# Optimization experiments

Hardware: AMD Instinct MI355X
Metric: run time of the kernel (lower is better)

Reference implementation:

```python
import jax, jax.numpy as jnp
import numpy as np

B, S, C, H = 2, 4096, 1024, 16
DH = C // H  # 64
# diffusers: attn.scale = dim_head ** -0.5; code divides scores by scale**0.5
SCALE = 1.0 / (float(DH) ** -0.25)  # == DH ** 0.25


def setup_inputs() -> dict:
    key = jax.random.key(0)
    ks = jax.random.split(key, 6)
    w = 0.02
    return {
        "hidden_states": jax.random.normal(ks[0], (B, S, C), jnp.float32),
        "Wq": jax.random.normal(ks[1], (C, C), jnp.float32) * w,
        "Wk": jax.random.normal(ks[2], (C, C), jnp.float32) * w,
        "Wv": jax.random.normal(ks[3], (C, C), jnp.float32) * w,
        "Wo": jax.random.normal(ks[4], (C, C), jnp.float32) * w,
        "bo": jnp.zeros((C,), jnp.float32),
        # token sizes >= 1 (number of patches each token represents)
        "token_sizes": jax.random.randint(ks[5], (B, S), 1, 17, jnp.int32),
    }


def _split_heads(x):
    # [B, S, C] -> [B, H, S, DH]
    return x.reshape(B, S, H, DH).transpose(0, 2, 1, 3)


def reference(hidden_states, Wq, Wk, Wv, Wo, bo, token_sizes):
    q = _split_heads(hidden_states @ Wq)  # [B,H,S,DH]
    k = _split_heads(hidden_states @ Wk)
    v = _split_heads(hidden_states @ Wv)
    # QK^T with diffusers-style scaling: scores / attn.scale**0.5 == scores * DH**0.25
    scores = jnp.einsum("bhqd,bhkd->bhqk", q, k) * SCALE  # [B,H,S,S]
    # additive log(token_size) bias over keys (self-attention path)
    log_sizes = jnp.log(token_sizes.astype(jnp.float32))  # [B,S]
    scores = scores + log_sizes[:, None, None, :]
    probs = jax.nn.softmax(scores, axis=-1)
    out = jnp.einsum("bhqk,bhkd->bhqd", probs, v)  # [B,H,S,DH]
    out = out.transpose(0, 2, 1, 3).reshape(B, S, C)  # merge heads
    return out @ Wo + bo  # to_out[0] linear; to_out[1] dropout is identity
```

## Files before the change

### kernel.cpp

```cpp
#include <hip/hip_runtime.h>


typedef unsigned short u16;
typedef unsigned int u32;
typedef _Float16 f16x8 __attribute__((ext_vector_type(8)));
typedef float f32x4 __attribute__((ext_vector_type(4)));
typedef short short4v __attribute__((ext_vector_type(4)));

constexpr int SEQ = 4096, CDIM = 1024, NH = 16, DHE = 64;
constexpr float SCALE2 = 2.8284271247461903f * 1.4426950408889634f;

union Frag { f16x8 v; short4v h[2]; };

__device__ __forceinline__ u16 f2h(float f) {
  union { _Float16 h; u16 u; } x;
  x.h = (_Float16)f;
  return x.u;
}

__device__ __forceinline__ u32 pkrtz(float a, float b) {
  u32 r;
  asm("v_cvt_pkrtz_f16_f32 %0, %1, %2" : "=v"(r) : "v"(a), "v"(b));
  return r;
}

__device__ __forceinline__ short4v pk4(const f32x4& v) {
  union { u32 w[2]; short4v s; } u;
  u.w[0] = pkrtz(v[0], v[1]);
  u.w[1] = pkrtz(v[2], v[3]);
  return u.s;
}

__device__ __forceinline__ float exp2fast(float x) {
  float r;
  asm("v_exp_f32 %0, %1" : "=v"(r) : "v"(x));
  return r;
}

__device__ __forceinline__ f32x4 mfma16(const Frag& a, const Frag& b, f32x4 c) {
  return __builtin_amdgcn_mfma_f32_16x16x32_f16(a.v, b.v, c, 0, 0, 0);
}


__global__ void cast_x_kernel(const float* __restrict__ x, u16* __restrict__ out) {
  size_t i = ((size_t)blockIdx.x * 256 + threadIdx.x) * 8;
  float4 a = *(const float4*)(x + i);
  float4 b = *(const float4*)(x + i + 4);
  uint4 o;
  o.x = (u32)f2h(a.x) | ((u32)f2h(a.y) << 16);
  o.y = (u32)f2h(a.z) | ((u32)f2h(a.w) << 16);
  o.z = (u32)f2h(b.x) | ((u32)f2h(b.y) << 16);
  o.w = (u32)f2h(b.z) | ((u32)f2h(b.w) << 16);
  *(uint4*)(out + i) = o;
}

__global__ __launch_bounds__(256) void transpose_w4_kernel(
    const float* __restrict__ Wq, const float* __restrict__ Wk,
    const float* __restrict__ Wv, const float* __restrict__ Wo,
    u16* __restrict__ dq, u16* __restrict__ dk,
    u16* __restrict__ dv, u16* __restrict__ dow) {
  __shared__ float tile[64][65];
  const float* src;
  u16* dst;
  switch (blockIdx.z) {
    case 0: src = Wq; dst = dq; break;
    case 1: src = Wk; dst = dk; break;
    case 2: src = Wv; dst = dv; break;
    default: src = Wo; dst = dow; break;
  }
  const int r0 = blockIdx.y * 64, c0 = blockIdx.x * 64;
  const int tx = threadIdx.x & 63, ty = threadIdx.x >> 6;
#pragma unroll
  for (int i = 0; i < 16; ++i) {
    const int row = i * 4 + ty;
    tile[row][tx] = src[(size_t)(r0 + row) * 1024 + c0 + tx];
  }
  __syncthreads();
#pragma unroll
  for (int i = 0; i < 16; ++i) {
    const int row = i * 4 + ty;
    dst[(size_t)(c0 + row) * 1024 + r0 + tx] = f2h(tile[tx][row]);
  }
}

__global__ void tscast_kernel(const int* __restrict__ ts, u16* __restrict__ out) {
  int i = blockIdx.x * 256 + threadIdx.x;
  out[i] = f2h((float)ts[i]);
}


template <int EPI>
__global__ __launch_bounds__(256) void gemm_f16(const u16* __restrict__ A,
                                                const u16* __restrict__ Bt,
                                                void* __restrict__ Out,
                                                const float* __restrict__ bias,
                                                const int* __restrict__ ts) {
  __shared__ __align__(16) short Alds[128][40];
  __shared__ __align__(16) short Blds[128][40];
  const int t = threadIdx.x;
  const int bnb = blockIdx.x;
  const int bm = blockIdx.y;
  const int lane = t & 63, wv = t >> 6;
  const int wm = wv >> 1, wn = wv & 1;
  const int l16 = lane & 15, lq = lane >> 4;

  f32x4 acc[4][4];
  f32x4 z = {0.f, 0.f, 0.f, 0.f};
#pragma unroll
  for (int i = 0; i < 4; ++i)
#pragma unroll
    for (int j = 0; j < 4; ++j) acc[i][j] = z;

  const int srow = (t * 8) >> 5;
  const int scol = (t * 8) & 31;

  for (int kb = 0; kb < 32; ++kb) {
    const int k0 = kb * 32;
#pragma unroll
    for (int i = 0; i < 2; ++i) {
      const int row = srow + i * 64;
      uint4 va = *(const uint4*)(A + (size_t)(bm * 128 + row) * 1024 + k0 + scol);
      *(uint4*)&Alds[row][scol] = va;
      uint4 vb = *(const uint4*)(Bt + (size_t)(bnb * 128 + row) * 1024 + k0 + scol);
      *(uint4*)&Blds[row][scol] = vb;
    }
    __syncthreads();

    Frag af[4], bf[4];
#pragma unroll
    for (int am = 0; am < 4; ++am) {
      const short* p = &Alds[wm * 64 + am * 16 + l16][lq * 4];
      af[am].h[0] = *(const short4v*)p;
      af[am].h[1] = *(const short4v*)(p + 16);
    }
#pragma unroll
    for (int bn = 0; bn < 4; ++bn) {
      const short* p = &Blds[wn * 64 + bn * 16 + l16][lq * 4];
      bf[bn].h[0] = *(const short4v*)p;
      bf[bn].h[1] = *(const short4v*)(p + 16);
    }
#pragma unroll
    for (int am = 0; am < 4; ++am)
#pragma unroll
      for (int bn = 0; bn < 4; ++bn) acc[am][bn] = mfma16(af[am], bf[bn], acc[am][bn]);
    __syncthreads();
  }

#pragma unroll
  for (int am = 0; am < 4; ++am) {
#pragma unroll
    for (int bn = 0; bn < 4; ++bn) {
#pragma unroll
      for (int r = 0; r < 4; ++r) {
        const int m = bm * 128 + wm * 64 + am * 16 + lq * 4 + r;
        const int n = bnb * 128 + wn * 64 + bn * 16 + l16;
        float vsum = acc[am][bn][r];
        if (EPI == 0) {
          const int which = n >> 10;
          const int nn = n & 1023;
          const int h = nn >> 6, d = nn & 63;
          const int b = m >> 12, s = m & 4095;
          const int bhh = b * NH + h;
          size_t addr;
          if (which == 2) {
            vsum *= (float)ts[b * SEQ + s];
            addr = (size_t)2 * 8388608 + ((size_t)bhh * DHE + d) * SEQ + s;
          } else {
            if (which == 0) vsum *= SCALE2;
            addr = (size_t)which * 8388608 + ((size_t)bhh * SEQ + s) * DHE + d;
          }
          ((u16*)Out)[addr] = f2h(vsum);
        } else {
          ((float*)Out)[(size_t)m * 1024 + n] = vsum + bias[n];
        }
      }
    }
  }
}


__global__ __launch_bounds__(256, 2) void attn_kernel(const u16* __restrict__ Q,
                                                      const u16* __restrict__ K,
                                                      const u16* __restrict__ Vt,
                                                      const u16* __restrict__ ts16,
                                                      u16* __restrict__ Out) {
  __shared__ __align__(16) short Klds[2][64][72];
  __shared__ __align__(16) short Vtlds[2][64][72];

  const int t = threadIdx.x;
  const int bh = blockIdx.x >> 4;
  const int qb = blockIdx.x & 15;
  const int lane = t & 63, wv = t >> 6;
  const int l16 = lane & 15, lq = lane >> 4;
  const int b = bh >> 4, h = bh & 15;

  Frag qf[4][2];
#pragma unroll
  for (int qh = 0; qh < 4; ++qh) {
    const int qrow = qb * 256 + wv * 64 + qh * 16 + l16;
    const u16* qp = Q + ((size_t)bh * SEQ + qrow) * DHE;
#pragma unroll
    for (int f = 0; f < 2; ++f) {
      qf[qh][f].h[0] = *(const short4v*)(qp + f * 32 + lq * 4);
      qf[qh][f].h[1] = *(const short4v*)(qp + f * 32 + lq * 4 + 16);
    }
  }

  float mrow[4] = {0.f, 0.f, 0.f, 0.f};
  f32x4 lsum[4];
  f32x4 oacc[4][4];
  f32x4 z = {0.f, 0.f, 0.f, 0.f};
#pragma unroll
  for (int qh = 0; qh < 4; ++qh) {
    lsum[qh] = z;
#pragma unroll
    for (int d = 0; d < 4; ++d) oacc[qh][d] = z;
  }

  const int a7 = t & 7, sd = a7 * 8, skey = t >> 3;
  const int vd = t >> 2, voct = (t & 3) * 8;
  const int vsw = ((vd >> 3) & 7) << 3;

  const u16* Kbase = K + (size_t)bh * SEQ * DHE;
  const u16* Vtbase = Vt + ((size_t)bh * DHE + vd) * SEQ;
  const u16* tsb = ts16 + b * SEQ;

  uint4 kv0 = *(const uint4*)(Kbase + (size_t)skey * DHE + sd);
  uint4 kv1 = *(const uint4*)(Kbase + (size_t)(skey + 32) * DHE + sd);
  uint4 vv0 = *(const uint4*)(Vtbase + voct);
  uint4 vv1 = *(const uint4*)(Vtbase + voct + 32);

  for (int kt = 0; kt < 64; ++kt) {
    short (*Kb)[72] = Klds[kt & 1];
    short (*Vb)[72] = Vtlds[kt & 1];
    *(uint4*)&Kb[skey][sd] = kv0;
    *(uint4*)&Kb[skey + 32][sd] = kv1;
    *(uint4*)&Vb[vd][voct ^ vsw] = vv0;
    *(uint4*)&Vb[vd][(voct + 32) ^ vsw] = vv1;

    if (kt < 63) {
      const u16* Kn = Kbase + (size_t)(kt + 1) * 64 * DHE + (size_t)skey * DHE + sd;
      kv0 = *(const uint4*)(Kn);
      kv1 = *(const uint4*)(Kn + 32 * DHE);
      const u16* Vn = Vtbase + (kt + 1) * 64 + voct;
      vv0 = *(const uint4*)(Vn);
      vv1 = *(const uint4*)(Vn + 32);
    }
    __syncthreads();

    Frag tsfr[2];
    {
      const u16* tst = tsb + kt * 64;
#pragma unroll
      for (int kh = 0; kh < 2; ++kh) {
        tsfr[kh].h[0] = *(const short4v*)(tst + kh * 32 + lq * 4);
        tsfr[kh].h[1] = *(const short4v*)(tst + kh * 32 + lq * 4 + 16);
      }
    }

    Frag kfr[4][2];
#pragma unroll
    for (int k2 = 0; k2 < 4; ++k2) {
#pragma unroll
      for (int f = 0; f < 2; ++f) {
        const short* p = &Kb[k2 * 16 + l16][f * 32 + lq * 4];
        kfr[k2][f].h[0] = *(const short4v*)p;
        kfr[k2][f].h[1] = *(const short4v*)(p + 16);
      }
    }

    Frag paf[4][2];
#pragma unroll
    for (int qh = 0; qh < 4; ++qh) {
      f32x4 seed;
      {
        const float nm = -mrow[qh];
        seed[0] = nm; seed[1] = nm; seed[2] = nm; seed[3] = nm;
      }
      f32x4 sc[4];
#pragma unroll
      for (int k2 = 0; k2 < 4; ++k2) {
        f32x4 a = mfma16(kfr[k2][0], qf[qh][0], seed);
        a = mfma16(kfr[k2][1], qf[qh][1], a);
        sc[k2] = a;
      }
      float hm[4];
#pragma unroll
      for (int k2 = 0; k2 < 4; ++k2) {
        const f32x4 s = sc[k2];
        hm[k2] = fmaxf(fmaxf(s[0], s[1]), fmaxf(s[2], s[3]));
      }
      float mx = fmaxf(fmaxf(hm[0], hm[1]), fmaxf(hm[2], hm[3]));
      mx = fmaxf(mx, __shfl_xor(mx, 16));
      mx = fmaxf(mx, __shfl_xor(mx, 32));
      if (__any(mx > 8.f)) {
        const float sh = fmaxf(mx, 0.f);
        const float al = exp2fast(-sh);
        mrow[qh] += sh;
        f32x4 alv;
#pragma unroll
        for (int r = 0; r < 4; ++r) alv[r] = __shfl(al, lq * 4 + r, 16);
#pragma unroll
        for (int dd = 0; dd < 4; ++dd) oacc[qh][dd] *= alv;
        lsum[qh] *= alv;
#pragma unroll
        for (int k2 = 0; k2 < 4; ++k2) sc[k2] -= sh;
      }
#pragma unroll
      for (int k2 = 0; k2 < 4; ++k2) {
        f32x4 s = sc[k2];
#pragma unroll
        for (int r = 0; r < 4; ++r) s[r] = exp2fast(s[r]);
        sc[k2] = s;
      }
      paf[qh][0].h[0] = pk4(sc[0]); paf[qh][0].h[1] = pk4(sc[1]);
      paf[qh][1].h[0] = pk4(sc[2]); paf[qh][1].h[1] = pk4(sc[3]);
      lsum[qh] = mfma16(paf[qh][0], tsfr[0], lsum[qh]);
      lsum[qh] = mfma16(paf[qh][1], tsfr[1], lsum[qh]);
    }

    __builtin_amdgcn_s_setprio(1);
#pragma unroll
    for (int dd = 0; dd < 4; ++dd) {
      const int vrow = dd * 16 + l16;
      const int e = ((vrow >> 3) & 7) << 3;
#pragma unroll
      for (int kh = 0; kh < 2; ++kh) {
        Frag vb;
        vb.h[0] = *(const short4v*)&Vb[vrow][(kh * 32 + lq * 4) ^ e];
        vb.h[1] = *(const short4v*)&Vb[vrow][(kh * 32 + 16 + lq * 4) ^ e];
#pragma unroll
        for (int qh = 0; qh < 4; ++qh)
          oacc[qh][dd] = mfma16(paf[qh][kh], vb, oacc[qh][dd]);
      }
    }
    __builtin_amdgcn_s_setprio(0);
  }

#pragma unroll
  for (int qh = 0; qh < 4; ++qh) {
    f32x4 linv;
#pragma unroll
    for (int r = 0; r < 4; ++r) linv[r] = 1.f / lsum[qh][r];
#pragma unroll
    for (int dd = 0; dd < 4; ++dd) {
#pragma unroll
      for (int r = 0; r < 4; ++r) {
        const int row = qb * 256 + wv * 64 + qh * 16 + lq * 4 + r;
        const float v = oacc[qh][dd][r] * linv[r];
        Out[((size_t)b * SEQ + row) * CDIM + h * DHE + dd * 16 + l16] = f2h(v);
      }
    }
  }
}


extern "C" void kernel_launch(void* const* d_in, const int* in_sizes, int n_in,
                              void* d_out, int out_size, void* d_ws, size_t ws_size,
                              hipStream_t stream) {
  const float* hs = (const float*)d_in[0];
  const float* Wq = (const float*)d_in[1];
  const float* Wk = (const float*)d_in[2];
  const float* Wv = (const float*)d_in[3];
  const float* Wo = (const float*)d_in[4];
  const float* bo = (const float*)d_in[5];
  const int* ts = (const int*)d_in[6];
  float* out = (float*)d_out;

  char* ws = (char*)d_ws;
  u16* xf = (u16*)(ws);
  u16* wtq = (u16*)(ws + 16777216);
  u16* wtk = (u16*)(ws + 18874368);
  u16* wtv = (u16*)(ws + 20971520);
  u16* wto = (u16*)(ws + 23068672);
  u16* qbuf = (u16*)(ws + 25165824);
  u16* kbuf = (u16*)(ws + 41943040);
  u16* vtbuf = (u16*)(ws + 58720256);
  u16* ts16 = (u16*)(ws + 75497472);

  cast_x_kernel<<<4096, 256, 0, stream>>>(hs, xf);
  transpose_w4_kernel<<<dim3(16, 16, 4), 256, 0, stream>>>(Wq, Wk, Wv, Wo,
                                                           wtq, wtk, wtv, wto);
  tscast_kernel<<<32, 256, 0, stream>>>(ts, ts16);

  gemm_f16<0><<<dim3(24, 64), 256, 0, stream>>>(xf, wtq, (void*)qbuf, nullptr, ts);

  attn_kernel<<<512, 256, 0, stream>>>(qbuf, kbuf, vtbuf, ts16, xf);

  gemm_f16<1><<<dim3(8, 64), 256, 0, stream>>>(xf, wto, (void*)out, bo, nullptr);

  (void)in_sizes; (void)n_in; (void)out_size; (void)ws_size;
}
```

Measured before the change: 339.5 us.

## Use direct global-to-LDS loads with XOR swizzle and interleave QK/softmax-PV

Replaces register-staged global loads with global_load_lds DMA directly into unpadded, XOR-swizzled shared memory in both the projection GEMM and the attention kernel, which removes VGPR staging and the LDS write instructions. The attention loop is restructured to issue the next tile's DMA after the barrier. It also interleaves the QK MFMAs of one query group with the softmax and PV work of the previous group to overlap matrix and vector work. V fragments are now reloaded per query group, adding LDS reads, and the GEMM has no double buffering, so its loads stay exposed.

```diff
diff --git a/kernel.cpp b/kernel.cpp
--- a/kernel.cpp
+++ b/kernel.cpp
@@ -10,6 +10,8 @@
 constexpr int SEQ = 4096, CDIM = 1024, NH = 16, DHE = 64;
 constexpr float SCALE2 = 2.8284271247461903f * 1.4426950408889634f;
 
+template <int N> struct IC { static constexpr int v = N; };
+
 union Frag { f16x8 v; short4v h[2]; };
 
 __device__ __forceinline__ u16 f2h(float f) {
@@ -39,6 +41,12 @@
 
 __device__ __forceinline__ f32x4 mfma16(const Frag& a, const Frag& b, f32x4 c) {
   return __builtin_amdgcn_mfma_f32_16x16x32_f16(a.v, b.v, c, 0, 0, 0);
+}
+
+__device__ __forceinline__ void gl16(const void* g, void* l) {
+  __builtin_amdgcn_global_load_lds(
+      (const __attribute__((address_space(1))) u32*)g,
+      (__attribute__((address_space(3))) u32*)l, 16, 0, 0);
 }
 
 
@@ -95,8 +103,8 @@
                                                 void* __restrict__ Out,
                                                 const float* __restrict__ bias,
                                                 const int* __restrict__ ts) {
-  __shared__ __align__(16) short Alds[128][40];
-  __shared__ __align__(16) short Blds[128][40];
+  __shared__ __align__(16) short Alds[128 * 32];
+  __shared__ __align__(16) short Blds[128 * 32];
   const int t = threadIdx.x;
   const int bnb = blockIdx.x;
   const int bm = blockIdx.y;
@@ -111,33 +119,37 @@
 #pragma unroll
     for (int j = 0; j < 4; ++j) acc[i][j] = z;
 
-  const int srow = (t * 8) >> 5;
-  const int scol = (t * 8) & 31;
+  const int srow = t >> 2;
+  const int schunk = (t & 3) ^ ((t >> 3) & 3);
+  const u16* Ag = A + (size_t)(bm * 128 + srow) * 1024 + schunk * 8;
+  const u16* Bg = Bt + (size_t)(bnb * 128 + srow) * 1024 + schunk * 8;
+  short* Ad = Alds + (t >> 6) * 512;
+  short* Bd = Blds + (t >> 6) * 512;
+
+  const int m2 = (l16 >> 1) & 3;
+  const int o0 = (((lq >> 1) ^ m2) * 8) + (lq & 1) * 4;
+  const int o1 = ((((lq >> 1) | 2) ^ m2) * 8) + (lq & 1) * 4;
 
   for (int kb = 0; kb < 32; ++kb) {
     const int k0 = kb * 32;
-#pragma unroll
-    for (int i = 0; i < 2; ++i) {
-      const int row = srow + i * 64;
-      uint4 va = *(const uint4*)(A + (size_t)(bm * 128 + row) * 1024 + k0 + scol);
-      *(uint4*)&Alds[row][scol] = va;
-      uint4 vb = *(const uint4*)(Bt + (size_t)(bnb * 128 + row) * 1024 + k0 + scol);
-      *(uint4*)&Blds[row][scol] = vb;
-    }
+    gl16(Ag + k0, Ad);
+    gl16(Ag + 64 * 1024 + k0, Ad + 2048);
+    gl16(Bg + k0, Bd);
+    gl16(Bg + 64 * 1024 + k0, Bd + 2048);
     __syncthreads();
 
     Frag af[4], bf[4];
 #pragma unroll
     for (int am = 0; am < 4; ++am) {
-      const short* p = &Alds[wm * 64 + am * 16 + l16][lq * 4];
-      af[am].h[0] = *(const short4v*)p;
-      af[am].h[1] = *(const short4v*)(p + 16);
+      const short* p = Alds + (wm * 64 + am * 16 + l16) * 32;
+      af[am].h[0] = *(const short4v*)(p + o0);
+      af[am].h[1] = *(const short4v*)(p + o1);
     }
 #pragma unroll
     for (int bn = 0; bn < 4; ++bn) {
-      const short* p = &Blds[wn * 64 + bn * 16 + l16][lq * 4];
-      bf[bn].h[0] = *(const short4v*)p;
-      bf[bn].h[1] = *(const short4v*)(p + 16);
+      const short* p = Blds + (wn * 64 + bn * 16 + l16) * 32;
+      bf[bn].h[0] = *(const short4v*)(p + o0);
+      bf[bn].h[1] = *(const short4v*)(p + o1);
     }
 #pragma unroll
     for (int am = 0; am < 4; ++am)
@@ -184,8 +196,8 @@
                                                       const u16* __restrict__ Vt,
                                                       const u16* __restrict__ ts16,
                                                       u16* __restrict__ Out) {
-  __shared__ __align__(16) short Klds[2][64][72];
-  __shared__ __align__(16) short Vtlds[2][64][72];
+  __shared__ __align__(16) short Klds[2][64 * 64];
+  __shared__ __align__(16) short Vlds[2][64 * 64];
 
   const int t = threadIdx.x;
   const int bh = blockIdx.x >> 4;
@@ -194,6 +206,25 @@
   const int l16 = lane & 15, lq = lane >> 4;
   const int b = bh >> 4, h = bh & 15;
 
+  const int arow = t >> 3;
+  const int achunk = (t & 7) ^ ((t >> 3) & 7);
+  const u16* Kg = K + ((size_t)bh * SEQ + arow) * DHE + achunk * 8;
+  const u16* Vg = Vt + ((size_t)bh * DHE + arow) * SEQ + achunk * 8;
+  const u16* tsb = ts16 + b * SEQ;
+
+  auto stage = [&](int tile, int bufi) {
+    short* Kd = &Klds[bufi][0] + (t >> 6) * 512;
+    short* Vd = &Vlds[bufi][0] + (t >> 6) * 512;
+    const u16* ks = Kg + (size_t)tile * 64 * 64;
+    const u16* vs = Vg + tile * 64;
+    gl16(ks, Kd);
+    gl16(ks + 32 * 64, Kd + 2048);
+    gl16(vs, Vd);
+    gl16(vs + (size_t)32 * SEQ, Vd + 2048);
+  };
+
+  stage(0, 0);
+
   Frag qf[4][2];
 #pragma unroll
   for (int qh = 0; qh < 4; ++qh) {
@@ -217,38 +248,84 @@
     for (int d = 0; d < 4; ++d) oacc[qh][d] = z;
   }
 
-  const int a7 = t & 7, sd = a7 * 8, skey = t >> 3;
-  const int vd = t >> 2, voct = (t & 3) * 8;
-  const int vsw = ((vd >> 3) & 7) << 3;
-
-  const u16* Kbase = K + (size_t)bh * SEQ * DHE;
-  const u16* Vtbase = Vt + ((size_t)bh * DHE + vd) * SEQ;
-  const u16* tsb = ts16 + b * SEQ;
-
-  uint4 kv0 = *(const uint4*)(Kbase + (size_t)skey * DHE + sd);
-  uint4 kv1 = *(const uint4*)(Kbase + (size_t)(skey + 32) * DHE + sd);
-  uint4 vv0 = *(const uint4*)(Vtbase + voct);
-  uint4 vv1 = *(const uint4*)(Vtbase + voct + 32);
+  const int m8 = l16 & 7;
+  const int sA = lq >> 1;
+  const int w4 = (lq & 1) * 4;
+  auto fr_ld = [&](Frag& fr, const short* base, int row, int fk) {
+    const short* p = base + row * 64;
+    const int sl = fk * 4 + sA;
+    fr.h[0] = *(const short4v*)(p + ((sl ^ m8) * 8 + w4));
+    fr.h[1] = *(const short4v*)(p + (((sl | 2) ^ m8) * 8 + w4));
+  };
+
+  Frag tsfr[2];
+
+  auto qk = [&](auto qc, Frag (&kf)[4][2], f32x4 (&dst)[4]) {
+    constexpr int qh = decltype(qc)::v;
+    const float nm = -mrow[qh];
+    f32x4 seed = {nm, nm, nm, nm};
+#pragma unroll
+    for (int k2 = 0; k2 < 4; ++k2) {
+      f32x4 a = mfma16(kf[k2][0], qf[qh][0], seed);
+      dst[k2] = mfma16(kf[k2][1], qf[qh][1], a);
+    }
+  };
+
+  auto smpv = [&](auto qc, const short* Vb, f32x4 (&sc)[4]) {
+    constexpr int qh = decltype(qc)::v;
+    float hm[4];
+#pragma unroll
+    for (int k2 = 0; k2 < 4; ++k2) {
+      const f32x4 s = sc[k2];
+      hm[k2] = fmaxf(fmaxf(s[0], s[1]), fmaxf(s[2], s[3]));
+    }
+    float mx = fmaxf(fmaxf(hm[0], hm[1]), fmaxf(hm[2], hm[3]));
+    mx = fmaxf(mx, __shfl_xor(mx, 16));
+    mx = fmaxf(mx, __shfl_xor(mx, 32));
+    if (__any(mx > 8.f)) {
+      const float sh = fmaxf(mx, 0.f);
+      const float al = exp2fast(-sh);
+      mrow[qh] += sh;
+      f32x4 alv;
+#pragma unroll
+      for (int r = 0; r < 4; ++r) alv[r] = __shfl(al, lq * 4 + r, 16);
+#pragma unroll
+      for (int dd = 0; dd < 4; ++dd) oacc[qh][dd] *= alv;
+      lsum[qh] *= alv;
+#pragma unroll
+      for (int k2 = 0; k2 < 4; ++k2) sc[k2] -= sh;
+    }
+#pragma unroll
+    for (int k2 = 0; k2 < 4; ++k2) {
+      f32x4 s = sc[k2];
+#pragma unroll
+      for (int r = 0; r < 4; ++r) s[r] = exp2fast(s[r]);
+      sc[k2] = s;
+    }
+    Frag paf0, paf1;
+    paf0.h[0] = pk4(sc[0]); paf0.h[1] = pk4(sc[1]);
+    paf1.h[0] = pk4(sc[2]); paf1.h[1] = pk4(sc[3]);
+    __builtin_amdgcn_s_setprio(1);
+    lsum[qh] = mfma16(paf0, tsfr[0], lsum[qh]);
+    lsum[qh] = mfma16(paf1, tsfr[1], lsum[qh]);
+#pragma unroll
+    for (int dd = 0; dd < 4; ++dd) {
+      Frag vb0, vb1;
+      fr_ld(vb0, Vb, dd * 16 + l16, 0);
+      fr_ld(vb1, Vb, dd * 16 + l16, 1);
+      oacc[qh][dd] = mfma16(paf0, vb0, oacc[qh][dd]);
+      oacc[qh][dd] = mfma16(paf1, vb1, oacc[qh][dd]);
+    }
+    __builtin_amdgcn_s_setprio(0);
+  };
+
+  f32x4 scA[4], scB[4];
 
   for (int kt = 0; kt < 64; ++kt) {
-    short (*Kb)[72] = Klds[kt & 1];
-    short (*Vb)[72] = Vtlds[kt & 1];
-    *(uint4*)&Kb[skey][sd] = kv0;
-    *(uint4*)&Kb[skey + 32][sd] = kv1;
-    *(uint4*)&Vb[vd][voct ^ vsw] = vv0;
-    *(uint4*)&Vb[vd][(voct + 32) ^ vsw] = vv1;
-
-    if (kt < 63) {
-      const u16* Kn = Kbase + (size_t)(kt + 1) * 64 * DHE + (size_t)skey * DHE + sd;
-      kv0 = *(const uint4*)(Kn);
-      kv1 = *(const uint4*)(Kn + 32 * DHE);
-      const u16* Vn = Vtbase + (kt + 1) * 64 + voct;
-      vv0 = *(const uint4*)(Vn);
-      vv1 = *(const uint4*)(Vn + 32);
-    }
     __syncthreads();
-
-    Frag tsfr[2];
+    const short* Kb = &Klds[kt & 1][0];
+    const short* Vb = &Vlds[kt & 1][0];
+
     {
       const u16* tst = tsb + kt * 64;
 #pragma unroll
@@ -257,84 +334,20 @@
         tsfr[kh].h[1] = *(const short4v*)(tst + kh * 32 + lq * 4 + 16);
       }
     }
+    if (kt < 63) stage(kt + 1, (kt + 1) & 1);
 
     Frag kfr[4][2];
 #pragma unroll
     for (int k2 = 0; k2 < 4; ++k2) {
-#pragma unroll
-      for (int f = 0; f < 2; ++f) {
-        const short* p = &Kb[k2 * 16 + l16][f * 32 + lq * 4];
-        kfr[k2][f].h[0] = *(const short4v*)p;
-        kfr[k2][f].h[1] = *(const short4v*)(p + 16);
-      }
-    }
-
-    Frag paf[4][2];
-#pragma unroll
-    for (int qh = 0; qh < 4; ++qh) {
-      f32x4 seed;
-      {
-        const float nm = -mrow[qh];
-        seed[0] = nm; seed[1] = nm; seed[2] = nm; seed[3] = nm;
-      }
-      f32x4 sc[4];
-#pragma unroll
-      for (int k2 = 0; k2 < 4; ++k2) {
-        f32x4 a = mfma16(kfr[k2][0], qf[qh][0], seed);
-        a = mfma16(kfr[k2][1], qf[qh][1], a);
-        sc[k2] = a;
-      }
-      float hm[4];
-#pragma unroll
-      for (int k2 = 0; k2 < 4; ++k2) {
-        const f32x4 s = sc[k2];
-        hm[k2] = fmaxf(fmaxf(s[0], s[1]), fmaxf(s[2], s[3]));
-      }
-      float mx = fmaxf(fmaxf(hm[0], hm[1]), fmaxf(hm[2], hm[3]));
-      mx = fmaxf(mx, __shfl_xor(mx, 16));
-      mx = fmaxf(mx, __shfl_xor(mx, 32));
-      if (__any(mx > 8.f)) {
-        const float sh = fmaxf(mx, 0.f);
-        const float al = exp2fast(-sh);
-        mrow[qh] += sh;
-        f32x4 alv;
-#pragma unroll
-        for (int r = 0; r < 4; ++r) alv[r] = __shfl(al, lq * 4 + r, 16);
-#pragma unroll
-        for (int dd = 0; dd < 4; ++dd) oacc[qh][dd] *= alv;
-        lsum[qh] *= alv;
-#pragma unroll
-        for (int k2 = 0; k2 < 4; ++k2) sc[k2] -= sh;
-      }
-#pragma unroll
-      for (int k2 = 0; k2 < 4; ++k2) {
-        f32x4 s = sc[k2];
-#pragma unroll
-        for (int r = 0; r < 4; ++r) s[r] = exp2fast(s[r]);
-        sc[k2] = s;
-      }
-      paf[qh][0].h[0] = pk4(sc[0]); paf[qh][0].h[1] = pk4(sc[1]);
-      paf[qh][1].h[0] = pk4(sc[2]); paf[qh][1].h[1] = pk4(sc[3]);
-      lsum[qh] = mfma16(paf[qh][0], tsfr[0], lsum[qh]);
-      lsum[qh] = mfma16(paf[qh][1], tsfr[1], lsum[qh]);
-    }
-
-    __builtin_amdgcn_s_setprio(1);
-#pragma unroll
-    for (int dd = 0; dd < 4; ++dd) {
-      const int vrow = dd * 16 + l16;
-      const int e = ((vrow >> 3) & 7) << 3;
-#pragma unroll
-      for (int kh = 0; kh < 2; ++kh) {
-        Frag vb;
-        vb.h[0] = *(const short4v*)&Vb[vrow][(kh * 32 + lq * 4) ^ e];
-        vb.h[1] = *(const short4v*)&Vb[vrow][(kh * 32 + 16 + lq * 4) ^ e];
-#pragma unroll
-        for (int qh = 0; qh < 4; ++qh)
-          oacc[qh][dd] = mfma16(paf[qh][kh], vb, oacc[qh][dd]);
-      }
-    }
-    __builtin_amdgcn_s_setprio(0);
+      fr_ld(kfr[k2][0], Kb, k2 * 16 + l16, 0);
+      fr_ld(kfr[k2][1], Kb, k2 * 16 + l16, 1);
+    }
+
+    qk(IC<0>{}, kfr, scA);
+    qk(IC<1>{}, kfr, scB);  smpv(IC<0>{}, Vb, scA);
+    qk(IC<2>{}, kfr, scA);  smpv(IC<1>{}, Vb, scB);
+    qk(IC<3>{}, kfr, scB);  smpv(IC<2>{}, Vb, scA);
+    smpv(IC<3>{}, Vb, scB);
   }
 
 #pragma unroll
```

Result: slower. 374.8 us (+10.4%).

## Use direct global-to-LDS loads in GEMM and interleave QK/softmax per query block

Applied to the files above, without the earlier changes.

The projection GEMM now loads A/B tiles straight into LDS with global_load_lds and a packed, XOR-swizzled layout, replacing register staging and padded rows. Fragment reads use matching swizzled offsets to avoid bank conflicts. In attention, the per-query-block QK MFMAs and softmax are split into lambdas and software-pipelined across two score buffers, so the next block's MFMAs can overlap the current block's exp/max work. This adds register pressure from the second score buffer, and correctness relies on the swizzle mapping matching between writes and reads.

```diff
diff --git a/kernel.cpp b/kernel.cpp
--- a/kernel.cpp
+++ b/kernel.cpp
@@ -10,6 +10,8 @@
 constexpr int SEQ = 4096, CDIM = 1024, NH = 16, DHE = 64;
 constexpr float SCALE2 = 2.8284271247461903f * 1.4426950408889634f;
 
+template <int N> struct IC { static constexpr int v = N; };
+
 union Frag { f16x8 v; short4v h[2]; };
 
 __device__ __forceinline__ u16 f2h(float f) {
@@ -39,6 +41,12 @@
 
 __device__ __forceinline__ f32x4 mfma16(const Frag& a, const Frag& b, f32x4 c) {
   return __builtin_amdgcn_mfma_f32_16x16x32_f16(a.v, b.v, c, 0, 0, 0);
+}
+
+__device__ __forceinline__ void gl16(const void* g, void* l) {
+  __builtin_amdgcn_global_load_lds(
+      (const __attribute__((address_space(1))) u32*)g,
+      (__attribute__((address_space(3))) u32*)l, 16, 0, 0);
 }
 
 
@@ -95,8 +103,8 @@
                                                 void* __restrict__ Out,
                                                 const float* __restrict__ bias,
                                                 const int* __restrict__ ts) {
-  __shared__ __align__(16) short Alds[128][40];
-  __shared__ __align__(16) short Blds[128][40];
+  __shared__ __align__(16) short Alds[128 * 32];
+  __shared__ __align__(16) short Blds[128 * 32];
   const int t = threadIdx.x;
   const int bnb = blockIdx.x;
   const int bm = blockIdx.y;
@@ -111,33 +119,37 @@
 #pragma unroll
     for (int j = 0; j < 4; ++j) acc[i][j] = z;
 
-  const int srow = (t * 8) >> 5;
-  const int scol = (t * 8) & 31;
+  const int srow = t >> 2;
+  const int schunk = (t & 3) ^ ((t >> 3) & 3);
+  const u16* Ag = A + (size_t)(bm * 128 + srow) * 1024 + schunk * 8;
+  const u16* Bg = Bt + (size_t)(bnb * 128 + srow) * 1024 + schunk * 8;
+  short* Ad = Alds + (t >> 6) * 512;
+  short* Bd = Blds + (t >> 6) * 512;
+
+  const int m2 = (l16 >> 1) & 3;
+  const int o0 = (((lq >> 1) ^ m2) * 8) + (lq & 1) * 4;
+  const int o1 = ((((lq >> 1) | 2) ^ m2) * 8) + (lq & 1) * 4;
 
   for (int kb = 0; kb < 32; ++kb) {
     const int k0 = kb * 32;
-#pragma unroll
-    for (int i = 0; i < 2; ++i) {
-      const int row = srow + i * 64;
-      uint4 va = *(const uint4*)(A + (size_t)(bm * 128 + row) * 1024 + k0 + scol);
-      *(uint4*)&Alds[row][scol] = va;
-      uint4 vb = *(const uint4*)(Bt + (size_t)(bnb * 128 + row) * 1024 + k0 + scol);
-      *(uint4*)&Blds[row][scol] = vb;
-    }
+    gl16(Ag + k0, Ad);
+    gl16(Ag + 64 * 1024 + k0, Ad + 2048);
+    gl16(Bg + k0, Bd);
+    gl16(Bg + 64 * 1024 + k0, Bd + 2048);
     __syncthreads();
 
     Frag af[4], bf[4];
 #pragma unroll
     for (int am = 0; am < 4; ++am) {
-      const short* p = &Alds[wm * 64 + am * 16 + l16][lq * 4];
-      af[am].h[0] = *(const short4v*)p;
-      af[am].h[1] = *(const short4v*)(p + 16);
+      const short* p = Alds + (wm * 64 + am * 16 + l16) * 32;
+      af[am].h[0] = *(const short4v*)(p + o0);
+      af[am].h[1] = *(const short4v*)(p + o1);
     }
 #pragma unroll
     for (int bn = 0; bn < 4; ++bn) {
-      const short* p = &Blds[wn * 64 + bn * 16 + l16][lq * 4];
-      bf[bn].h[0] = *(const short4v*)p;
-      bf[bn].h[1] = *(const short4v*)(p + 16);
+      const short* p = Blds + (wn * 64 + bn * 16 + l16) * 32;
+      bf[bn].h[0] = *(const short4v*)(p + o0);
+      bf[bn].h[1] = *(const short4v*)(p + o1);
     }
 #pragma unroll
     for (int am = 0; am < 4; ++am)
@@ -230,6 +242,10 @@
   uint4 vv0 = *(const uint4*)(Vtbase + voct);
   uint4 vv1 = *(const uint4*)(Vtbase + voct + 32);
 
+  Frag tsfr[2];
+  Frag paf[4][2];
+  f32x4 scA[4], scB[4];
+
   for (int kt = 0; kt < 64; ++kt) {
     short (*Kb)[72] = Klds[kt & 1];
     short (*Vb)[72] = Vtlds[kt & 1];
@@ -248,7 +264,6 @@
     }
     __syncthreads();
 
-    Frag tsfr[2];
     {
       const u16* tst = tsb + kt * 64;
 #pragma unroll
@@ -269,21 +284,19 @@
       }
     }
 
-    Frag paf[4][2];
-#pragma unroll
-    for (int qh = 0; qh < 4; ++qh) {
-      f32x4 seed;
-      {
-        const float nm = -mrow[qh];
-        seed[0] = nm; seed[1] = nm; seed[2] = nm; seed[3] = nm;
-      }
-      f32x4 sc[4];
+    auto qkq = [&](auto qc, f32x4 (&sc)[4]) {
+      constexpr int qh = decltype(qc)::v;
+      const float nm = -mrow[qh];
+      f32x4 seed = {nm, nm, nm, nm};
 #pragma unroll
       for (int k2 = 0; k2 < 4; ++k2) {
         f32x4 a = mfma16(kfr[k2][0], qf[qh][0], seed);
-        a = mfma16(kfr[k2][1], qf[qh][1], a);
-        sc[k2] = a;
-      }
+        sc[k2] = mfma16(kfr[k2][1], qf[qh][1], a);
+      }
+    };
+
+    auto smq = [&](auto qc, f32x4 (&sc)[4]) {
+      constexpr int qh = decltype(qc)::v;
       float hm[4];
 #pragma unroll
       for (int k2 = 0; k2 < 4; ++k2) {
@@ -317,7 +330,16 @@
       paf[qh][1].h[0] = pk4(sc[2]); paf[qh][1].h[1] = pk4(sc[3]);
       lsum[qh] = mfma16(paf[qh][0], tsfr[0], lsum[qh]);
       lsum[qh] = mfma16(paf[qh][1], tsfr[1], lsum[qh]);
-    }
+    };
+
+    qkq(IC<0>{}, scA);
+    qkq(IC<1>{}, scB);
+    smq(IC<0>{}, scA);
+    qkq(IC<2>{}, scA);
+    smq(IC<1>{}, scB);
+    qkq(IC<3>{}, scB);
+    smq(IC<2>{}, scA);
+    smq(IC<3>{}, scB);
 
     __builtin_amdgcn_s_setprio(1);
 #pragma unroll
```

Result: faster. 328.6 us (-3.2%).
